# Kernel optimization log

Hardware: AMD Instinct MI355X
Metric: run time of the kernel (lower is better)

The kernel has to match this reference:

```python
import jax, jax.numpy as jnp
import numpy as np

EPS = 1e-5
K = 16
DILATION = 1

def _bn(x, g, b, axes):
    # BatchNorm in training mode: batch statistics over all axes except channel (last)
    m = jnp.mean(x, axis=axes, keepdims=True)
    v = jnp.var(x, axis=axes, keepdims=True)
    return (x - m) * jax.lax.rsqrt(v + EPS) * g + b

def _knn_idx(p, q, k):
    # p: [B,N,3], q: [B,M,3] -> indices [B,M,k] of nearest points in p for each q
    d = (jnp.sum(q * q, -1)[:, :, None]
         - 2.0 * jnp.einsum('bmc,bnc->bmn', q, p)
         + jnp.sum(p * p, -1)[:, None, :])  # [B,M,N]
    _, idx = jax.lax.top_k(-d, k)
    return jax.lax.stop_gradient(idx)

def setup_inputs() -> dict:
    key = jax.random.key(0)
    ks = jax.random.split(key, 16)
    B, N, M, Cin, Cout = 8, 8192, 2048, 64, 128
    mid, K2 = Cout // 4, K * K
    s = 0.02
    d = {
        'p': jax.random.normal(ks[0], (B, N, 3), jnp.float32),
        'q': jax.random.normal(ks[1], (B, M, 3), jnp.float32),
        'x': jax.random.normal(ks[2], (B, Cin, N), jnp.float32),
        # mlp: two 1x1 convs (3->mid->mid) each with BN
        'W1': jax.random.normal(ks[3], (mid, 3), jnp.float32) * s,
        'b1': jnp.zeros((mid,), jnp.float32),
        'g1': jnp.ones((mid,), jnp.float32), 'be1': jnp.zeros((mid,), jnp.float32),
        'W2': jax.random.normal(ks[4], (mid, mid), jnp.float32) * s,
        'b2': jnp.zeros((mid,), jnp.float32),
        'g2': jnp.ones((mid,), jnp.float32), 'be2': jnp.zeros((mid,), jnp.float32),
        # stn: conv [1,K] (3->K^2), then two 1x1 convs (K^2->K^2)
        'Ws1': jax.random.normal(ks[5], (K2, 3, K), jnp.float32) * s,
        'bs1': jnp.zeros((K2,), jnp.float32),
        'gs1': jnp.ones((K2,), jnp.float32), 'bes1': jnp.zeros((K2,), jnp.float32),
        'Ws2': jax.random.normal(ks[6], (K2, K2), jnp.float32) * s,
        'bs2': jnp.zeros((K2,), jnp.float32),
        'gs2': jnp.ones((K2,), jnp.float32), 'bes2': jnp.zeros((K2,), jnp.float32),
        'Ws3': jax.random.normal(ks[7], (K2, K2), jnp.float32) * s,
        'bs3': jnp.zeros((K2,), jnp.float32),
        # final conv [1,K]: (Cin+mid -> Cout) with BN
        'Wc': jax.random.normal(ks[8], (Cout, Cin + mid, K), jnp.float32) * s,
        'bc': jnp.zeros((Cout,), jnp.float32),
        'gc': jnp.ones((Cout,), jnp.float32), 'bec': jnp.zeros((Cout,), jnp.float32),
    }
    return d

def reference(p, q, x, W1, b1, g1, be1, W2, b2, g2, be2,
              Ws1, bs1, gs1, bes1, Ws2, bs2, gs2, bes2, Ws3, bs3,
              Wc, bc, gc, bec):
    B, M = q.shape[0], q.shape[1]
    idx = _knn_idx(p, q, K * DILATION)[..., ::DILATION]  # [B,M,K]
    # gather neighbor coords and center: p_hat [B,M,K,3]
    p_n = jax.vmap(lambda a, i: a[i])(p, idx)
    p_hat = p_n - q[:, :, None, :]
    # mlp (pointwise convs, channel-last)
    h = jax.nn.relu(_bn(jnp.einsum('bmkc,oc->bmko', p_hat, W1) + b1, g1, be1, (0, 1, 2)))
    h = jax.nn.relu(_bn(jnp.einsum('bmkc,oc->bmko', h, W2) + b2, g2, be2, (0, 1, 2)))
    # gather features: x [B,Cin,N] -> [B,M,K,Cin]
    xt = jnp.transpose(x, (0, 2, 1))
    x_n = jax.vmap(lambda a, i: a[i])(xt, idx)
    x_hat = jnp.concatenate([h, x_n], axis=-1)  # [B,M,K,mid+Cin]
    # stn -> transform T [B,M,K,K]
    t = jax.nn.relu(_bn(jnp.einsum('bmkc,ock->bmo', p_hat, Ws1) + bs1, gs1, bes1, (0, 1)))
    t = jax.nn.relu(_bn(jnp.einsum('bmi,oi->bmo', t, Ws2) + bs2, gs2, bes2, (0, 1)))
    t = jnp.einsum('bmi,oi->bmo', t, Ws3) + bs3  # [B,M,K*K]
    T = t.reshape(B, M, K, K)
    x2 = jnp.einsum('bmij,bmjc->bmic', T, x_hat)  # [B,M,K,mid+Cin]
    out = jax.nn.relu(_bn(jnp.einsum('bmkc,ock->bmo', x2, Wc) + bc, gc, bec, (0, 1)))  # [B,M,Cout]
    return (q, jnp.transpose(out, (0, 2, 1)))  # q, x:[B,Cout,M]
```

## Files before the change

kernel.cpp:

```cpp
#include <hip/hip_runtime.h>
#include <hip/hip_bf16.h>


#define EPS 1e-5f

constexpr int Bb   = 8;
constexpr int Np   = 8192;
constexpr int Mq   = 2048;
constexpr int COUT = 128;
constexpr int BM   = Bb * Mq;
constexpr int BMK  = BM * 16;
constexpr int GC   = 16;
constexpr int NC   = GC * GC * GC;
constexpr int CAP  = 320;

typedef __attribute__((ext_vector_type(8))) short short8;
typedef __attribute__((ext_vector_type(4))) float f32x4;

__device__ __forceinline__ unsigned short f2bf(float x) {
  unsigned u = __float_as_uint(x);
  u += 0x7fffu + ((u >> 16) & 1u);
  return (unsigned short)(u >> 16);
}
__device__ __forceinline__ float bf2f_lo(unsigned v) { return __uint_as_float(v << 16); }
__device__ __forceinline__ float bf2f_hi(unsigned v) { return __uint_as_float(v & 0xffff0000u); }

__device__ __forceinline__ int cell_of(float c) {
  int v = (int)floorf(c * 2.0f + 8.0f);
  return v < 0 ? 0 : (v > 15 ? 15 : v);
}

__device__ __forceinline__ unsigned enc_dist(float d) {
  unsigned uu = __float_as_uint(d);
  return uu ^ (((unsigned)(((int)uu) >> 31)) | 0x80000000u);
}

__device__ __forceinline__ void bsort64(unsigned long long& v, int lane) {
#pragma unroll
  for (int k = 2; k <= 64; k <<= 1) {
#pragma unroll
    for (int jj = k >> 1; jj > 0; jj >>= 1) {
      unsigned long long o = __shfl_xor(v, jj);
      bool keepMin = (((lane & k) == 0) == ((lane & jj) == 0));
      unsigned long long mn = v < o ? v : o;
      unsigned long long mx = v < o ? o : v;
      v = keepMin ? mn : mx;
    }
  }
}
__device__ __forceinline__ void bmerge64(unsigned long long& v, int lane) {
#pragma unroll
  for (int jj = 32; jj > 0; jj >>= 1) {
    unsigned long long o = __shfl_xor(v, jj);
    bool keepMin = ((lane & jj) == 0);
    unsigned long long mn = v < o ? v : o;
    unsigned long long mx = v < o ? o : v;
    v = keepMin ? mn : mx;
  }
}
__device__ __forceinline__ unsigned long long sort_smallest64(const unsigned long long* buf,
                                                              int C, int lane) {
  unsigned long long run = (lane < C) ? buf[lane] : ~0ULL;
  bsort64(run, lane);
  for (int b2 = 64; b2 < C; b2 += 64) {
    unsigned long long v = (b2 + lane < C) ? buf[b2 + lane] : ~0ULL;
    bsort64(v, lane);
    unsigned long long vr = __shfl_xor(v, 63);
    unsigned long long m = run < vr ? run : vr;
    bmerge64(m, lane);
    run = m;
  }
  return run;
}


__device__ __forceinline__ void bn1_compute(int o, const float* __restrict__ st,
                                            const float* __restrict__ W1,
                                            const float* __restrict__ b1,
                                            const float* __restrict__ g1,
                                            const float* __restrict__ be1,
                                            float* sc_out, float* shf_out) {
  float n = (float)BMK;
  float w0 = W1[3 * o], w1 = W1[3 * o + 1], w2 = W1[3 * o + 2], b = b1[o];
  float s0 = st[0], s1 = st[1], s2 = st[2];
  float m00 = st[3], m11 = st[4], m22 = st[5], m01 = st[6], m02 = st[7], m12 = st[8];
  float ws = (w0 * s0 + w1 * s1 + w2 * s2) / n;
  float mean = b + ws;
  float quad = w0 * w0 * m00 + w1 * w1 * m11 + w2 * w2 * m22 +
               2.f * (w0 * w1 * m01 + w0 * w2 * m02 + w1 * w2 * m12);
  float ex2 = quad / n + 2.f * b * ws + b * b;
  float var = ex2 - mean * mean;
  float sc = g1[o] * rsqrtf(var + EPS);
  *sc_out = sc;
  *shf_out = be1[o] - mean * sc + b * sc;
}

__global__ __launch_bounds__(256) void prep_kernel(const float* __restrict__ p,
                                                   const float* __restrict__ x,
                                                   const float* __restrict__ Wc,
                                                   const float* __restrict__ Ws1,
                                                   float4* __restrict__ pp4,
                                                   float* __restrict__ xt,
                                                   unsigned short* __restrict__ wcrp,
                                                   unsigned short* __restrict__ ws1r,
                                                   int* __restrict__ hist) {
  __shared__ float tile[64][65];
  int blk = blockIdx.x;
  int tid = threadIdx.x;
  if (blk < 256) {
    int i = blk * 256 + tid;
    float px = p[3 * i], py = p[3 * i + 1], pz = p[3 * i + 2];
    float pp = __fadd_rn(__fadd_rn(__fmul_rn(px, px), __fmul_rn(py, py)), __fmul_rn(pz, pz));
    pp4[i] = make_float4(px, py, pz, pp);
    int b = i >> 13;
    int cid = (cell_of(px) << 8) | (cell_of(py) << 4) | cell_of(pz);
    atomicAdd(&hist[b * NC + cid], 1);
  } else if (blk < 1280) {
    int bx = blk - 256;
    int b = bx >> 7;
    int n0 = (bx & 127) << 6;
    int nl = tid & 63;
    int r0 = tid >> 6;
    const float* xb = x + (size_t)b * 64 * Np;
    for (int c = r0; c < 64; c += 4) tile[c][nl] = xb[(size_t)c * Np + n0 + nl];
    __syncthreads();
    float* xtb = xt + (size_t)b * Np * 64;
    for (int n = r0; n < 64; n += 4) xtb[(size_t)(n0 + n) * 64 + nl] = tile[nl][n];
  } else if (blk < 2048) {
    int g = (blk - 1280) * 256 + tid;
    if (g < 128 * 1536) {
      int o = g / 1536, r = g % 1536;
      int c = r % 96, j = r / 96;
      wcrp[g] = f2bf(Wc[(size_t)o * 1536 + c * 16 + j]);
    }
  } else {
    int g = (blk - 2048) * 256 + tid;
    int o = g >> 6, i = g & 63;
    float val = 0.f;
    if (i < 48) {
      int k = i / 3, c = i - 3 * k;
      val = Ws1[(size_t)o * 48 + c * 16 + k];
    }
    unsigned short h = f2bf(val);
    float hf = __uint_as_float(((unsigned)h) << 16);
    unsigned short l = f2bf(val - hf);
    ws1r[g] = h;
    ws1r[16384 + g] = l;
  }
}

__global__ __launch_bounds__(256) void prefix_kernel(const int* __restrict__ hist,
                                                     int* __restrict__ cellstart,
                                                     int* __restrict__ cursor) {
  __shared__ int ls[256];
  int b = blockIdx.x, t = threadIdx.x;
  const int* h = hist + b * NC;
  int loc[16], s = 0;
#pragma unroll
  for (int k = 0; k < 16; ++k) { loc[k] = h[t * 16 + k]; s += loc[k]; }
  ls[t] = s;
  __syncthreads();
  for (int off = 1; off < 256; off <<= 1) {
    int v = (t >= off) ? ls[t - off] : 0;
    __syncthreads();
    ls[t] += v;
    __syncthreads();
  }
  int run = ls[t] - s;
  int* cs = cellstart + b * (NC + 1);
  int* cu = cursor + b * NC;
#pragma unroll
  for (int k = 0; k < 16; ++k) {
    cs[t * 16 + k] = run;
    cu[t * 16 + k] = run;
    run += loc[k];
  }
  if (t == 255) cs[NC] = run;
}

__global__ __launch_bounds__(256) void scatter_kernel(const float4* __restrict__ pp4,
                                                      int* __restrict__ cursor,
                                                      float4* __restrict__ sp4,
                                                      int* __restrict__ sidx) {
  int i = blockIdx.x * 256 + threadIdx.x;
  int b = i >> 13;
  float4 pv = pp4[i];
  int cid = (cell_of(pv.x) << 8) | (cell_of(pv.y) << 4) | cell_of(pv.z);
  int pos = atomicAdd(&cursor[b * NC + cid], 1);
  sp4[(size_t)b * Np + pos] = pv;
  sidx[(size_t)b * Np + pos] = i & 8191;
}

__global__ __launch_bounds__(256) void knn_kernel(const float4* __restrict__ pp4,
                                                  const float4* __restrict__ sp4,
                                                  const int* __restrict__ cellstart,
                                                  const float* __restrict__ q,
                                                  int* __restrict__ idx_out) {
  __shared__ unsigned long long cand[8][CAP];
  int tid = threadIdx.x;
  int wslot = tid >> 6;
  int wave = blockIdx.x * 4 + wslot;
  int lane = tid & 63;
  int q0 = wave * 2;
  int b = q0 >> 11;
  const float4* pb = pp4 + (size_t)b * Np;
  const float4* sp = sp4 + (size_t)b * Np;
  const int* cs = cellstart + b * (NC + 1);
  float qx[2], qy[2], qz[2], qqv[2];
#pragma unroll
  for (int j = 0; j < 2; ++j) {
    const float* qp = q + (size_t)(q0 + j) * 3;
    qx[j] = qp[0]; qy[j] = qp[1]; qz[j] = qp[2];
    qqv[j] = __fadd_rn(__fadd_rn(__fmul_rn(qx[j], qx[j]), __fmul_rn(qy[j], qy[j])),
                       __fmul_rn(qz[j], qz[j]));
  }
  float tau_f[2] = {INFINITY, INFINITY};

  for (int j = 0; j < 2; ++j) {
    int cx = cell_of(qx[j]), cy = cell_of(qy[j]), cz = cell_of(qz[j]);
    int alo = 0, blo = 0, nbw = 1, ncols = 1, zlo = 0, zhi = 0;
    int myS = 0, myE = 0;
    for (int r = 0;; ++r) {
      alo = cx - r; if (alo < 0) alo = 0;
      int ahi = cx + r; if (ahi > 15) ahi = 15;
      blo = cy - r; if (blo < 0) blo = 0;
      int bhi = cy + r; if (bhi > 15) bhi = 15;
      zlo = cz - r; if (zlo < 0) zlo = 0;
      zhi = cz + r; if (zhi > 15) zhi = 15;
      nbw = bhi - blo + 1;
      ncols = (ahi - alo + 1) * nbw;
      int total = 0;
      for (int l0 = 0; l0 < ncols; l0 += 64) {
        int l = l0 + lane;
        int sL = 0, eL = 0;
        if (l < ncols) {
          int da = l / nbw, db = l - da * nbw;
          int cbase = ((alo + da) << 8) | ((blo + db) << 4);
          sL = cs[cbase + zlo];
          eL = cs[cbase + zhi + 1];
        }
        if (l0 == 0) { myS = sL; myE = eL; }
        total += eL - sL;
      }
#pragma unroll
      for (int o = 32; o > 0; o >>= 1) total += __shfl_xor(total, o);
      if (total >= 16 || r >= 15) break;
    }
    unsigned u0 = 0xFFFFFFFFu, u1 = 0xFFFFFFFFu;
    int wcnt = 0;
    int ccen = (cx - alo) * nbw + (cy - blo);
    for (int c2 = 0; c2 < ncols && wcnt < 128; ++c2) {
      int cc = (c2 == 0) ? ccen : (c2 <= ccen ? c2 - 1 : c2);
      int s0, e;
      if (cc < 64) {
        s0 = __shfl(myS, cc);
        e = __shfl(myE, cc);
      } else {
        int da = cc / nbw, db = cc - da * nbw;
        int cbase = ((alo + da) << 8) | ((blo + db) << 4);
        s0 = cs[cbase + zlo];
        e = cs[cbase + zhi + 1];
      }
      for (int off = s0; off < e && wcnt < 128; off += 64) {
        int rem = e - off; if (rem > 64) rem = 64;
        int rot = wcnt & 63;
        int rel = (lane - rot) & 63;
        int g = wcnt + rel;
        if (rel < rem && g < 128) {
          float4 pv = sp[off + rel];
          float ee = __fmaf_rn(qz[j], pv.z, __fmaf_rn(qy[j], pv.y, __fmul_rn(qx[j], pv.x)));
          float d = __fadd_rn(__fsub_rn(qqv[j], __fmul_rn(2.0f, ee)), pv.w);
          unsigned uu = enc_dist(d);
          if (g < 64) u0 = uu; else u1 = uu;
        }
        wcnt += rem;
      }
    }
    unsigned lo = 0u, hi = 0xFF800000u;
    for (int it = 0; it < 20; ++it) {
      unsigned mid = lo + ((hi - lo) >> 1);
      int c = (int)__popcll(__ballot(u0 <= mid)) + (int)__popcll(__ballot(u1 <= mid));
      if (c >= 16) hi = mid; else lo = mid + 1;
    }
    tau_f[j] = (hi >= 0x80000000u) ? __uint_as_float(hi ^ 0x80000000u)
                                   : __uint_as_float(~hi);
  }

  int cnt[2] = {0, 0};
  unsigned long long lanebelow = (1ULL << lane) - 1ULL;
  for (int base = 0; base < Np; base += 256) {
    float4 pv[4];
#pragma unroll
    for (int u4 = 0; u4 < 4; ++u4) pv[u4] = pb[base + u4 * 64 + lane];
    float d[4][2];
#pragma unroll
    for (int u4 = 0; u4 < 4; ++u4)
#pragma unroll
      for (int j = 0; j < 2; ++j) {
        float e = __fmaf_rn(qz[j], pv[u4].z, __fmaf_rn(qy[j], pv[u4].y, __fmul_rn(qx[j], pv[u4].x)));
        d[u4][j] = __fadd_rn(__fsub_rn(qqv[j], __fmul_rn(2.0f, e)), pv[u4].w);
      }
#pragma unroll
    for (int u4 = 0; u4 < 4; ++u4)
#pragma unroll
      for (int j = 0; j < 2; ++j) {
        unsigned long long mask = __ballot(d[u4][j] <= tau_f[j]);
        if (mask) {
          if (d[u4][j] <= tau_f[j]) {
            int i = base + u4 * 64 + lane;
            unsigned uu = enc_dist(d[u4][j]);
            int wp = cnt[j] + (int)__popcll(mask & lanebelow);
            if (wp < CAP)
              cand[wslot * 2 + j][wp] = (((unsigned long long)uu) << 32) | (unsigned)i;
          }
          cnt[j] += (int)__popcll(mask);
        }
      }
  }
  __syncthreads();

  for (int j = 0; j < 2; ++j) {
    int slot = wslot * 2 + j;
    if (cnt[j] <= CAP) {
      unsigned long long run = sort_smallest64(&cand[slot][0], cnt[j], lane);
      if (lane < 16)
        idx_out[(size_t)(q0 + j) * 16 + lane] = (int)(run & 0xffffffffULL);
    } else {
      unsigned long long kk = ~0ULL;
      float tl = tau_f[j];
      for (int base = 0; base < Np; base += 64) {
        float4 pv = pb[base + lane];
        float ee = __fmaf_rn(qz[j], pv.z, __fmaf_rn(qy[j], pv.y, __fmul_rn(qx[j], pv.x)));
        float dv = __fadd_rn(__fsub_rn(qqv[j], __fmul_rn(2.0f, ee)), pv.w);
        unsigned long long mask = __ballot(dv <= tl);
        if (mask) {
          unsigned uu = enc_dist(dv);
          unsigned long long cd = (((unsigned long long)uu) << 32) | (unsigned)(base + lane);
          do {
            int src = __ffsll((unsigned long long)mask) - 1;
            mask &= mask - 1;
            unsigned long long ck = __shfl(cd, src);
            unsigned long long up = __shfl_up(kk, 1);
            if (lane == 0) up = 0ULL;
            if (lane < 16 && ck < kk) kk = (up > ck) ? up : ck;
          } while (mask);
          unsigned long long tt = __shfl(kk, 15);
          unsigned tm = (unsigned)(tt >> 32);
          unsigned inv2 = tm ^ ((tm & 0x80000000u) ? 0x80000000u : 0xFFFFFFFFu);
          float tc = (tm == 0xFFFFFFFFu) ? INFINITY : __uint_as_float(inv2);
          if (tc < tl) tl = tc;
        }
      }
      if (lane < 16)
        idx_out[(size_t)(q0 + j) * 16 + lane] = (int)(kk & 0xffffffffULL);
    }
  }
}

__global__ __launch_bounds__(256) void phat_stats_kernel(const float4* __restrict__ pp4,
                                                         const float* __restrict__ q,
                                                         const int* __restrict__ idx,
                                                         float* __restrict__ phat,
                                                         float* __restrict__ stats) {
  float a[9];
#pragma unroll
  for (int k = 0; k < 9; ++k) a[k] = 0.f;
  int tid = threadIdx.x;
  for (int it = 0; it < 4; ++it) {
    int bmk = blockIdx.x * 256 + tid + it * 65536;
    int bm = bmk >> 4;
    int b = bm >> 11;
    int j = idx[bmk];
    float4 pv = pp4[(size_t)b * Np + j];
    const float* qp = q + (size_t)bm * 3;
    float h0 = pv.x - qp[0], h1 = pv.y - qp[1], h2 = pv.z - qp[2];
    phat[(size_t)bmk * 3 + 0] = h0;
    phat[(size_t)bmk * 3 + 1] = h1;
    phat[(size_t)bmk * 3 + 2] = h2;
    a[0] += h0; a[1] += h1; a[2] += h2;
    a[3] += h0 * h0; a[4] += h1 * h1; a[5] += h2 * h2;
    a[6] += h0 * h1; a[7] += h0 * h2; a[8] += h1 * h2;
  }
#pragma unroll
  for (int off = 32; off > 0; off >>= 1)
#pragma unroll
    for (int k = 0; k < 9; ++k) a[k] += __shfl_down(a[k], off);
  __shared__ float ls[9];
  if (tid < 9) ls[tid] = 0.f;
  __syncthreads();
  if ((tid & 63) == 0)
    for (int k = 0; k < 9; ++k) atomicAdd(&ls[k], a[k]);
  __syncthreads();
  if (tid < 9) atomicAdd(&stats[tid], ls[tid]);
}

__global__ __launch_bounds__(256) void stats2_kernel(const float* __restrict__ phat,
                                                     const float* __restrict__ stats,
                                                     const float* __restrict__ W1,
                                                     const float* __restrict__ b1,
                                                     const float* __restrict__ g1,
                                                     const float* __restrict__ be1,
                                                     const float* __restrict__ W2,
                                                     const float* __restrict__ b2,
                                                     float* __restrict__ stats2) {
  __shared__ float hsh[256 * 36];
  __shared__ float w2s[32 * 33];
  __shared__ float w1s[96], sc1[32], sh1[32], b2s[32], ls[64];
  int tid = threadIdx.x;
  if (tid < 32) {
    bn1_compute(tid, stats, W1, b1, g1, be1, &sc1[tid], &sh1[tid]);
    b2s[tid] = b2[tid];
  }
  if (tid < 96) w1s[tid] = W1[tid];
  if (tid < 64) ls[tid] = 0.f;
  for (int e = tid; e < 1024; e += 256) w2s[(e >> 5) * 33 + (e & 31)] = W2[e];
  __syncthreads();
  {
    int bmk = blockIdx.x * 256 + tid;
    float h0 = phat[(size_t)bmk * 3], hy = phat[(size_t)bmk * 3 + 1], hz = phat[(size_t)bmk * 3 + 2];
#pragma unroll
    for (int o4 = 0; o4 < 8; ++o4) {
      float4 r;
      float* rp = (float*)&r;
#pragma unroll
      for (int u = 0; u < 4; ++u) {
        int o = o4 * 4 + u;
        float t = w1s[3 * o] * h0 + w1s[3 * o + 1] * hy + w1s[3 * o + 2] * hz;
        rp[u] = fmaxf(0.f, t * sc1[o] + sh1[o]);
      }
      *(float4*)&hsh[tid * 36 + o4 * 4] = r;
    }
  }
  __syncthreads();
  int oc = tid & 31, grp = tid >> 5;
  float wrow[32];
#pragma unroll
  for (int c = 0; c < 32; ++c) wrow[c] = w2s[oc * 33 + c];
  float bias = b2s[oc];
  float ss = 0.f, qq = 0.f;
  for (int r = 0; r < 32; ++r) {
    int row = grp * 32 + r;
    float a = bias;
    const float4* hr = (const float4*)&hsh[row * 36];
#pragma unroll
    for (int c4 = 0; c4 < 8; ++c4) {
      float4 hv = hr[c4];
      a += hv.x * wrow[c4 * 4 + 0];
      a += hv.y * wrow[c4 * 4 + 1];
      a += hv.z * wrow[c4 * 4 + 2];
      a += hv.w * wrow[c4 * 4 + 3];
    }
    ss += a;
    qq += a * a;
  }
  atomicAdd(&ls[oc], ss);
  atomicAdd(&ls[32 + oc], qq);
  __syncthreads();
  if (tid < 64) atomicAdd(&stats2[tid], ls[tid]);
}

__global__ __launch_bounds__(256) void stn1_kernel(const float* __restrict__ phat,
                                                   const unsigned short* __restrict__ ws1r,
                                                   const float* __restrict__ bs1,
                                                   float* __restrict__ pt1,
                                                   float* __restrict__ spt1) {
  __shared__ unsigned short Ah[64 * 72], Al[64 * 72], Bh[128 * 72], Bl[128 * 72];
  __shared__ float ls[256];
  int tid = threadIdx.x;
  ls[tid] = 0.f;
  int mb = blockIdx.x >> 1, nb = blockIdx.x & 1;
  int bm0 = mb * 64, o0 = nb * 128;
  {
    int zr = tid >> 2, zc = 48 + (tid & 3) * 4;
    *(unsigned long long*)&Ah[zr * 72 + zc] = 0ULL;
    *(unsigned long long*)&Al[zr * 72 + zc] = 0ULL;
  }
  {
    int ar = tid >> 2, aseg = tid & 3;
    const float* Ap = phat + (size_t)(bm0 + ar) * 48 + aseg * 12;
    float4 v0 = *(const float4*)(Ap);
    float4 v1 = *(const float4*)(Ap + 4);
    float4 v2 = *(const float4*)(Ap + 8);
    float av[12] = {v0.x, v0.y, v0.z, v0.w, v1.x, v1.y, v1.z, v1.w, v2.x, v2.y, v2.z, v2.w};
    unsigned long long ph[3] = {0ULL, 0ULL, 0ULL}, pl[3] = {0ULL, 0ULL, 0ULL};
#pragma unroll
    for (int t = 0; t < 12; ++t) {
      unsigned short h = f2bf(av[t]);
      float hf = __uint_as_float(((unsigned)h) << 16);
      unsigned short l = f2bf(av[t] - hf);
      ph[t >> 2] |= ((unsigned long long)h) << ((t & 3) * 16);
      pl[t >> 2] |= ((unsigned long long)l) << ((t & 3) * 16);
    }
    int base = ar * 72 + aseg * 12;
#pragma unroll
    for (int t4 = 0; t4 < 3; ++t4) {
      *(unsigned long long*)&Ah[base + t4 * 4] = ph[t4];
      *(unsigned long long*)&Al[base + t4 * 4] = pl[t4];
    }
  }
#pragma unroll
  for (int pass = 0; pass < 4; ++pass) {
    int g = pass * 2048 + tid * 8;
    int br = g >> 6, i2 = g & 63;
    short8 vh = *(const short8*)&ws1r[(size_t)(o0 + br) * 64 + i2];
    short8 vl = *(const short8*)&ws1r[16384 + (size_t)(o0 + br) * 64 + i2];
    *(short8*)&Bh[br * 72 + i2] = vh;
    *(short8*)&Bl[br * 72 + i2] = vl;
  }
  __syncthreads();
  int wid = tid >> 6, lane = tid & 63;
  int wm = wid >> 1, wn = wid & 1;
  int mh = lane & 15, quad = lane >> 4;
  f32x4 acc[2][4];
#pragma unroll
  for (int a = 0; a < 2; ++a)
#pragma unroll
    for (int bq = 0; bq < 4; ++bq) acc[a][bq] = (f32x4){0.f, 0.f, 0.f, 0.f};
#pragma unroll
  for (int kc = 0; kc < 2; ++kc) {
    int ko = kc * 32 + quad * 8;
#pragma unroll
    for (int mt = 0; mt < 2; ++mt) {
      short8 ah = *(const short8*)&Ah[(wm * 32 + mt * 16 + mh) * 72 + ko];
      short8 al = *(const short8*)&Al[(wm * 32 + mt * 16 + mh) * 72 + ko];
#pragma unroll
      for (int nt = 0; nt < 4; ++nt) {
        short8 bh = *(const short8*)&Bh[(wn * 64 + nt * 16 + mh) * 72 + ko];
        short8 bl = *(const short8*)&Bl[(wn * 64 + nt * 16 + mh) * 72 + ko];
        acc[mt][nt] = __builtin_amdgcn_mfma_f32_16x16x32_bf16(ah, bh, acc[mt][nt], 0, 0, 0);
        acc[mt][nt] = __builtin_amdgcn_mfma_f32_16x16x32_bf16(ah, bl, acc[mt][nt], 0, 0, 0);
        acc[mt][nt] = __builtin_amdgcn_mfma_f32_16x16x32_bf16(al, bh, acc[mt][nt], 0, 0, 0);
      }
    }
  }
#pragma unroll
  for (int mt = 0; mt < 2; ++mt)
#pragma unroll
    for (int nt = 0; nt < 4; ++nt) {
      int colL = wn * 64 + nt * 16 + mh;
      int col = o0 + colL;
      float bvv = bs1[col];
      float ps = 0.f, pq = 0.f;
#pragma unroll
      for (int r = 0; r < 4; ++r) {
        float val = acc[mt][nt][r] + bvv;
        pt1[(size_t)(bm0 + wm * 32 + mt * 16 + quad * 4 + r) * 256 + col] = val;
        ps += val;
        pq += val * val;
      }
      atomicAdd(&ls[colL], ps);
      atomicAdd(&ls[128 + colL], pq);
    }
  __syncthreads();
  if (tid < 128) {
    atomicAdd(&spt1[o0 + tid], ls[tid]);
    atomicAdd(&spt1[256 + o0 + tid], ls[128 + tid]);
  }
}

__global__ __launch_bounds__(256) void stn_mm_kernel(const float* __restrict__ in,
                                                     const float* __restrict__ sums,
                                                     const float* __restrict__ gg,
                                                     const float* __restrict__ be,
                                                     const float* __restrict__ W,
                                                     const float* __restrict__ bias,
                                                     float* __restrict__ out,
                                                     float* __restrict__ outstats,
                                                     int do_stats) {
  __shared__ unsigned short As[64 * 40], Bs[128 * 40];
  __shared__ float scA[256], shA[256], ls[256];
  int tid = threadIdx.x;
  ls[tid] = 0.f;
  {
    float n = (float)BM;
    float mean = sums[tid] / n;
    float var = sums[256 + tid] / n - mean * mean;
    float s = gg[tid] * rsqrtf(var + EPS);
    scA[tid] = s;
    shA[tid] = be[tid] - mean * s;
  }
  int mb = blockIdx.x >> 1, nb = blockIdx.x & 1;
  int bm0 = mb * 64, o0 = nb * 128;
  int wid = tid >> 6, lane = tid & 63;
  int wm = wid >> 1, wn = wid & 1;
  int mh = lane & 15, quad = lane >> 4;
  f32x4 acc[2][4];
#pragma unroll
  for (int a = 0; a < 2; ++a)
#pragma unroll
    for (int bq = 0; bq < 4; ++bq) acc[a][bq] = (f32x4){0.f, 0.f, 0.f, 0.f};
  int ar = tid >> 2, aseg = tid & 3;
  const float* Ag = in + (size_t)(bm0 + ar) * 256 + aseg * 8;
  int aoff = ar * 40 + aseg * 8;
  int ci = aseg * 8;
  for (int i0 = 0; i0 < 256; i0 += 32) {
    __syncthreads();
    float4 v0 = *(const float4*)(Ag + i0);
    float4 v1 = *(const float4*)(Ag + i0 + 4);
    float av[8] = {v0.x, v0.y, v0.z, v0.w, v1.x, v1.y, v1.z, v1.w};
    short8 ap;
#pragma unroll
    for (int k = 0; k < 8; ++k)
      ap[k] = (short)f2bf(fmaxf(0.f, av[k] * scA[i0 + ci + k] + shA[i0 + ci + k]));
    *(short8*)&As[aoff] = ap;
#pragma unroll
    for (int jb = 0; jb < 2; ++jb) {
      int br = jb * 64 + ar;
      const float* Bg = W + (size_t)(o0 + br) * 256 + aseg * 8;
      float4 u0 = *(const float4*)(Bg + i0);
      float4 u1 = *(const float4*)(Bg + i0 + 4);
      float bv[8] = {u0.x, u0.y, u0.z, u0.w, u1.x, u1.y, u1.z, u1.w};
      short8 bp;
#pragma unroll
      for (int k = 0; k < 8; ++k) bp[k] = (short)f2bf(bv[k]);
      *(short8*)&Bs[br * 40 + aseg * 8] = bp;
    }
    __syncthreads();
#pragma unroll
    for (int mt = 0; mt < 2; ++mt) {
      short8 af = *(const short8*)&As[(wm * 32 + mt * 16 + mh) * 40 + quad * 8];
#pragma unroll
      for (int nt = 0; nt < 4; ++nt) {
        short8 bf = *(const short8*)&Bs[(wn * 64 + nt * 16 + mh) * 40 + quad * 8];
        acc[mt][nt] = __builtin_amdgcn_mfma_f32_16x16x32_bf16(af, bf, acc[mt][nt], 0, 0, 0);
      }
    }
  }
#pragma unroll
  for (int mt = 0; mt < 2; ++mt)
#pragma unroll
    for (int nt = 0; nt < 4; ++nt) {
      int colL = wn * 64 + nt * 16 + mh;
      int col = o0 + colL;
      float bvv = bias[col];
      float ps = 0.f, pq = 0.f;
#pragma unroll
      for (int r = 0; r < 4; ++r) {
        float val = acc[mt][nt][r] + bvv;
        out[(size_t)(bm0 + wm * 32 + mt * 16 + quad * 4 + r) * 256 + col] = val;
        ps += val;
        pq += val * val;
      }
      if (do_stats) {
        atomicAdd(&ls[colL], ps);
        atomicAdd(&ls[128 + colL], pq);
      }
    }
  if (do_stats) {
    __syncthreads();
    if (tid < 128) {
      atomicAdd(&outstats[o0 + tid], ls[tid]);
      atomicAdd(&outstats[256 + o0 + tid], ls[128 + tid]);
    }
  }
}

__global__ __launch_bounds__(256) void xhat_x2_kernel(const float* __restrict__ phat,
                                                      const float* __restrict__ stats,
                                                      const float* __restrict__ stats2,
                                                      const float* __restrict__ W1,
                                                      const float* __restrict__ b1,
                                                      const float* __restrict__ g1,
                                                      const float* __restrict__ be1,
                                                      const float* __restrict__ W2,
                                                      const float* __restrict__ b2,
                                                      const float* __restrict__ g2,
                                                      const float* __restrict__ be2,
                                                      const float* __restrict__ xt,
                                                      const int* __restrict__ idx,
                                                      const float* __restrict__ Tbuf,
                                                      unsigned short* __restrict__ x2) {
  __shared__ unsigned short xh[256 * 98];
  __shared__ float w1s[96], w2s[32 * 33], sc1[32], sh1[32], sc2[32], sh2[32];
  int tid = threadIdx.x;
  if (tid < 32) {
    bn1_compute(tid, stats, W1, b1, g1, be1, &sc1[tid], &sh1[tid]);
    float n = (float)BMK;
    float mean = stats2[tid] / n;
    float var = stats2[32 + tid] / n - mean * mean;
    float s = g2[tid] * rsqrtf(var + EPS);
    sc2[tid] = s;
    sh2[tid] = be2[tid] - mean * s + b2[tid] * s;
  }
  if (tid < 96) w1s[tid] = W1[tid];
  for (int e = tid; e < 1024; e += 256) w2s[(e >> 5) * 33 + (e & 31)] = W2[e];
  __syncthreads();
  int bm0 = blockIdx.x * 16;
  int b = bm0 >> 11;
  int bml = tid >> 4, j = tid & 15;
  int bmk = (bm0 + bml) * 16 + j;
  int row = tid * 98;
  {
    float h0 = phat[(size_t)bmk * 3], hy = phat[(size_t)bmk * 3 + 1], hz = phat[(size_t)bmk * 3 + 2];
    float h1[32];
#pragma unroll
    for (int o = 0; o < 32; ++o) {
      float t = w1s[3 * o] * h0 + w1s[3 * o + 1] * hy + w1s[3 * o + 2] * hz;
      h1[o] = fmaxf(0.f, t * sc1[o] + sh1[o]);
    }
#pragma unroll
    for (int o4 = 0; o4 < 8; ++o4) {
      float r[4];
#pragma unroll
      for (int u = 0; u < 4; ++u) {
        int o = o4 * 4 + u;
        float a = 0.f;
#pragma unroll
        for (int c = 0; c < 32; ++c) a += h1[c] * w2s[o * 33 + c];
        r[u] = fmaxf(0.f, a * sc2[o] + sh2[o]);
      }
      *(unsigned*)&xh[row + o4 * 4] = (unsigned)f2bf(r[0]) | (((unsigned)f2bf(r[1])) << 16);
      *(unsigned*)&xh[row + o4 * 4 + 2] = (unsigned)f2bf(r[2]) | (((unsigned)f2bf(r[3])) << 16);
    }
    int jx = idx[bmk];
    const float4* xr = (const float4*)(xt + ((size_t)b * Np + jx) * 64);
#pragma unroll
    for (int c4 = 0; c4 < 16; ++c4) {
      float4 v = xr[c4];
      *(unsigned*)&xh[row + 32 + c4 * 4] = (unsigned)f2bf(v.x) | (((unsigned)f2bf(v.y)) << 16);
      *(unsigned*)&xh[row + 32 + c4 * 4 + 2] = (unsigned)f2bf(v.z) | (((unsigned)f2bf(v.w)) << 16);
    }
  }
  float Tr[16];
  {
    const float4* tg = (const float4*)(Tbuf + (size_t)(bm0 + bml) * 256 + j * 16);
#pragma unroll
    for (int w4 = 0; w4 < 4; ++w4) {
      float4 tv = tg[w4];
      Tr[w4 * 4 + 0] = tv.x; Tr[w4 * 4 + 1] = tv.y;
      Tr[w4 * 4 + 2] = tv.z; Tr[w4 * 4 + 3] = tv.w;
    }
  }
  __syncthreads();
#pragma unroll
  for (int c0 = 0; c0 < 96; c0 += 32) {
    float acc[32];
#pragma unroll
    for (int cc = 0; cc < 32; ++cc) acc[cc] = 0.f;
#pragma unroll
    for (int jj = 0; jj < 16; ++jj) {
      const unsigned* xr2 = (const unsigned*)&xh[(bml * 16 + jj) * 98 + c0];
      float t = Tr[jj];
#pragma unroll
      for (int cc = 0; cc < 16; ++cc) {
        unsigned uv = xr2[cc];
        acc[cc * 2] += t * bf2f_lo(uv);
        acc[cc * 2 + 1] += t * bf2f_hi(uv);
      }
    }
    unsigned* dst = (unsigned*)(x2 + (size_t)bmk * 96 + c0);
#pragma unroll
    for (int cc = 0; cc < 16; ++cc)
      dst[cc] = (unsigned)f2bf(acc[cc * 2]) | (((unsigned)f2bf(acc[cc * 2 + 1])) << 16);
  }
}

__global__ __launch_bounds__(256) void preout_kernel(const unsigned short* __restrict__ x2,
                                                     const unsigned short* __restrict__ Wcrp,
                                                     const float* __restrict__ bc,
                                                     float* __restrict__ pout,
                                                     float* __restrict__ spout) {
  __shared__ unsigned short As[64 * 40], Bs[128 * 40];
  __shared__ float ls[256];
  int tid = threadIdx.x;
  ls[tid] = 0.f;
  int bm0 = blockIdx.x * 64;
  int wid = tid >> 6, lane = tid & 63;
  int wm = wid >> 1, wn = wid & 1;
  int mh = lane & 15, quad = lane >> 4;
  f32x4 acc[2][4];
#pragma unroll
  for (int a = 0; a < 2; ++a)
#pragma unroll
    for (int bq = 0; bq < 4; ++bq) acc[a][bq] = (f32x4){0.f, 0.f, 0.f, 0.f};
  int ar = tid >> 2, aseg = tid & 3;
  const unsigned short* Ag = x2 + (size_t)(bm0 + ar) * 1536 + aseg * 8;
  const unsigned short* Bg0 = Wcrp + (size_t)ar * 1536 + aseg * 8;
  const unsigned short* Bg1 = Wcrp + (size_t)(64 + ar) * 1536 + aseg * 8;
  int aoff = ar * 40 + aseg * 8;
  short8 a_pre = *(const short8*)Ag;
  short8 b_pre0 = *(const short8*)Bg0;
  short8 b_pre1 = *(const short8*)Bg1;
  for (int i0 = 0; i0 < 1536; i0 += 32) {
    __syncthreads();
    *(short8*)&As[aoff] = a_pre;
    *(short8*)&Bs[aoff] = b_pre0;
    *(short8*)&Bs[64 * 40 + aoff] = b_pre1;
    __syncthreads();
    if (i0 + 32 < 1536) {
      a_pre = *(const short8*)(Ag + i0 + 32);
      b_pre0 = *(const short8*)(Bg0 + i0 + 32);
      b_pre1 = *(const short8*)(Bg1 + i0 + 32);
    }
#pragma unroll
    for (int mt = 0; mt < 2; ++mt) {
      short8 af = *(const short8*)&As[(wm * 32 + mt * 16 + mh) * 40 + quad * 8];
#pragma unroll
      for (int nt = 0; nt < 4; ++nt) {
        short8 bf = *(const short8*)&Bs[(wn * 64 + nt * 16 + mh) * 40 + quad * 8];
        acc[mt][nt] = __builtin_amdgcn_mfma_f32_16x16x32_bf16(af, bf, acc[mt][nt], 0, 0, 0);
      }
    }
  }
#pragma unroll
  for (int mt = 0; mt < 2; ++mt)
#pragma unroll
    for (int nt = 0; nt < 4; ++nt) {
      int col = wn * 64 + nt * 16 + mh;
      float bvv = bc[col];
      float ps = 0.f, pq = 0.f;
#pragma unroll
      for (int r = 0; r < 4; ++r) {
        float val = acc[mt][nt][r] + bvv;
        pout[(size_t)(bm0 + wm * 32 + mt * 16 + quad * 4 + r) * 128 + col] = val;
        ps += val;
        pq += val * val;
      }
      atomicAdd(&ls[col], ps);
      atomicAdd(&ls[128 + col], pq);
    }
  __syncthreads();
  atomicAdd(&spout[tid], ls[tid]);
}

__global__ __launch_bounds__(256) void final_kernel(const float* __restrict__ q,
                                                    const float* __restrict__ pout,
                                                    const float* __restrict__ scs,
                                                    const float* __restrict__ gc,
                                                    const float* __restrict__ bec,
                                                    float* __restrict__ dout) {
  __shared__ float ldsT[128 * 65];
  int blk = blockIdx.x;
  int tid = threadIdx.x;
  if (blk < 192) {
    int g = blk * 256 + tid;
    dout[g] = q[g];
    return;
  }
  int blk2 = blk - 192;
  int b = blk2 >> 5;
  int m0 = (blk2 & 31) * 64;
  int row = tid >> 2, seg = tid & 3;
  const float4* src = (const float4*)(pout + ((size_t)(b * Mq) + m0 + row) * 128 + seg * 32);
#pragma unroll
  for (int k4 = 0; k4 < 8; ++k4) {
    float4 v = src[k4];
    int o = seg * 32 + k4 * 4;
    ldsT[(o + 0) * 65 + row] = v.x;
    ldsT[(o + 1) * 65 + row] = v.y;
    ldsT[(o + 2) * 65 + row] = v.z;
    ldsT[(o + 3) * 65 + row] = v.w;
  }
  __syncthreads();
  int lane = tid & 63, wv = tid >> 6;
  float n = (float)BM;
  float* base = dout + (size_t)BM * 3 + (size_t)b * COUT * Mq + m0;
#pragma unroll
  for (int rep = 0; rep < 32; ++rep) {
    int o = wv * 32 + rep;
    float mean = scs[o] / n;
    float var = scs[128 + o] / n - mean * mean;
    float s = gc[o] * rsqrtf(var + EPS);
    float shv = bec[o] - mean * s;
    float v = ldsT[o * 65 + lane];
    base[(size_t)o * Mq + lane] = fmaxf(0.f, v * s + shv);
  }
}

extern "C" void kernel_launch(void* const* d_in, const int* in_sizes, int n_in, void* d_out,
                              int out_size, void* d_ws, size_t ws_size, hipStream_t stream) {
  const float* p = (const float*)d_in[0];
  const float* q = (const float*)d_in[1];
  const float* x = (const float*)d_in[2];
  const float* W1 = (const float*)d_in[3];
  const float* b1 = (const float*)d_in[4];
  const float* g1 = (const float*)d_in[5];
  const float* be1 = (const float*)d_in[6];
  const float* W2 = (const float*)d_in[7];
  const float* b2 = (const float*)d_in[8];
  const float* g2 = (const float*)d_in[9];
  const float* be2 = (const float*)d_in[10];
  const float* Ws1 = (const float*)d_in[11];
  const float* bs1 = (const float*)d_in[12];
  const float* gs1 = (const float*)d_in[13];
  const float* bes1 = (const float*)d_in[14];
  const float* Ws2 = (const float*)d_in[15];
  const float* bs2 = (const float*)d_in[16];
  const float* gs2 = (const float*)d_in[17];
  const float* bes2 = (const float*)d_in[18];
  const float* Ws3 = (const float*)d_in[19];
  const float* bs3 = (const float*)d_in[20];
  const float* Wc = (const float*)d_in[21];
  const float* bc = (const float*)d_in[22];
  const float* gc = (const float*)d_in[23];
  const float* bec = (const float*)d_in[24];
  float* dout = (float*)d_out;

  char* ws = (char*)d_ws;
  float* stats = (float*)ws;
  size_t off = 8192;
  float4* pp4 = (float4*)(ws + off);  off += (size_t)Bb * Np * 16;
  int* idxb = (int*)(ws + off);       off += (size_t)BMK * 4;
  float* xt = (float*)(ws + off);     off += (size_t)Bb * Np * 64 * 4;
  float* phat = (float*)(ws + off);   off += (size_t)BMK * 3 * 4;
  float* pt1 = (float*)(ws + off);    off += (size_t)BM * 256 * 4;
  float* pt2 = (float*)(ws + off);    off += (size_t)BM * 256 * 4;
  float* Tb = (float*)(ws + off);     off += (size_t)BM * 256 * 4;
  float* pout = (float*)(ws + off);   off += (size_t)BM * 128 * 4;
  unsigned short* wcrp = (unsigned short*)(ws + off); off += (size_t)1536 * 128 * 2;
  unsigned short* x2 = (unsigned short*)(ws + off);   off += (size_t)BM * 1536 * 2;
  int* hist = (int*)(ws + off);       off += (size_t)Bb * NC * 4;
  int* cursor = (int*)(ws + off);     off += (size_t)Bb * NC * 4;
  int* cellstart = (int*)(ws + off);  off += (size_t)Bb * (NC + 1) * 4;
  float4* sp4 = (float4*)(ws + off);  off += (size_t)Bb * Np * 16;
  int* sidx = (int*)(ws + off);       off += (size_t)Bb * Np * 4;
  unsigned short* ws1r = (unsigned short*)(ws + off); off += (size_t)2 * 256 * 64 * 2;

  hipMemsetAsync(stats, 0, 8192, stream);
  hipMemsetAsync(hist, 0, (size_t)Bb * NC * 4, stream);
  hipLaunchKernelGGL(prep_kernel, dim3(2112), dim3(256), 0, stream, p, x, Wc, Ws1, pp4, xt, wcrp, ws1r, hist);
  hipLaunchKernelGGL(prefix_kernel, dim3(8), dim3(256), 0, stream, hist, cellstart, cursor);
  hipLaunchKernelGGL(scatter_kernel, dim3(256), dim3(256), 0, stream, pp4, cursor, sp4, sidx);
  hipLaunchKernelGGL(knn_kernel, dim3(2048), dim3(256), 0, stream, pp4, sp4, cellstart, q, idxb);
  hipLaunchKernelGGL(phat_stats_kernel, dim3(256), dim3(256), 0, stream, pp4, q, idxb, phat, stats);
  hipLaunchKernelGGL(stn1_kernel, dim3(512), dim3(256), 0, stream, phat, ws1r, bs1, pt1, stats + 128);
  hipLaunchKernelGGL(stats2_kernel, dim3(1024), dim3(256), 0, stream, phat, stats, W1, b1, g1, be1, W2, b2, stats + 16);
  hipLaunchKernelGGL(stn_mm_kernel, dim3(512), dim3(256), 0, stream, pt1, stats + 128, gs1, bes1, Ws2, bs2, pt2, stats + 640, 1);
  hipLaunchKernelGGL(stn_mm_kernel, dim3(512), dim3(256), 0, stream, pt2, stats + 640, gs2, bes2, Ws3, bs3, Tb, (float*)nullptr, 0);
  hipLaunchKernelGGL(xhat_x2_kernel, dim3(1024), dim3(256), 0, stream, phat, stats, stats + 16,
                     W1, b1, g1, be1, W2, b2, g2, be2, xt, idxb, Tb, x2);
  hipLaunchKernelGGL(preout_kernel, dim3(256), dim3(256), 0, stream, x2, wcrp, bc, pout, stats + 1152);
  hipLaunchKernelGGL(final_kernel, dim3(448), dim3(256), 0, stream, q, pout, stats + 1152, gc, bec, dout);
}
```

Baseline: 381.1 us.

## Restrict KNN candidate scan to grid cells within threshold radius; shrink xhat LDS

The second KNN pass no longer scans all 8192 points per query. It computes a radius from the per-query threshold and visits only the sorted grid cells inside that bounding box, then maps each hit back to its original index through sidx. Separately, xhat_x2 now stages one 32-channel chunk at a time into a smaller padded LDS buffer, keeping h2 in registers and loading the x gather per chunk. The first part should remove most of the brute-force distance work. The costs are reliance on the radius padding being conservative, per-column shuffle overhead, and extra block barriers in xhat_x2.

Measured after the change: 379.9 us. No clear change (-0.3%).

```diff
diff --git a/kernel.cpp b/kernel.cpp
--- a/kernel.cpp
+++ b/kernel.cpp
@@ -193,6 +193,7 @@
 
 __global__ __launch_bounds__(256) void knn_kernel(const float4* __restrict__ pp4,
                                                   const float4* __restrict__ sp4,
+                                                  const int* __restrict__ sidx,
                                                   const int* __restrict__ cellstart,
                                                   const float* __restrict__ q,
                                                   int* __restrict__ idx_out) {
@@ -205,6 +206,7 @@
   int b = q0 >> 11;
   const float4* pb = pp4 + (size_t)b * Np;
   const float4* sp = sp4 + (size_t)b * Np;
+  const int* sx = sidx + (size_t)b * Np;
   const int* cs = cellstart + b * (NC + 1);
   float qx[2], qy[2], qz[2], qqv[2];
 #pragma unroll
@@ -288,34 +290,51 @@
 
   int cnt[2] = {0, 0};
   unsigned long long lanebelow = (1ULL << lane) - 1ULL;
-  for (int base = 0; base < Np; base += 256) {
-    float4 pv[4];
-#pragma unroll
-    for (int u4 = 0; u4 < 4; ++u4) pv[u4] = pb[base + u4 * 64 + lane];
-    float d[4][2];
-#pragma unroll
-    for (int u4 = 0; u4 < 4; ++u4)
-#pragma unroll
-      for (int j = 0; j < 2; ++j) {
-        float e = __fmaf_rn(qz[j], pv[u4].z, __fmaf_rn(qy[j], pv[u4].y, __fmul_rn(qx[j], pv[u4].x)));
-        d[u4][j] = __fadd_rn(__fsub_rn(qqv[j], __fmul_rn(2.0f, e)), pv[u4].w);
-      }
-#pragma unroll
-    for (int u4 = 0; u4 < 4; ++u4)
-#pragma unroll
-      for (int j = 0; j < 2; ++j) {
-        unsigned long long mask = __ballot(d[u4][j] <= tau_f[j]);
+  for (int j = 0; j < 2; ++j) {
+    float R = sqrtf(fmaxf(tau_f[j], 0.f) + 3e-5f) * 1.0005f;
+    int ax0 = cell_of(qx[j] - R), ax1 = cell_of(qx[j] + R);
+    int ay0 = cell_of(qy[j] - R), ay1 = cell_of(qy[j] + R);
+    int az0 = cell_of(qz[j] - R), az1 = cell_of(qz[j] + R);
+    int nby = ay1 - ay0 + 1;
+    int ncols = (ax1 - ax0 + 1) * nby;
+    int myS = 0, myE = 0;
+    if (lane < ncols) {
+      int da = lane / nby, db = lane - da * nby;
+      int cbase = ((ax0 + da) << 8) | ((ay0 + db) << 4);
+      myS = cs[cbase + az0];
+      myE = cs[cbase + az1 + 1];
+    }
+    for (int cc = 0; cc < ncols; ++cc) {
+      int s0, e;
+      if (cc < 64) {
+        s0 = __shfl(myS, cc);
+        e = __shfl(myE, cc);
+      } else {
+        int da = cc / nby, db = cc - da * nby;
+        int cbase = ((ax0 + da) << 8) | ((ay0 + db) << 4);
+        s0 = cs[cbase + az0];
+        e = cs[cbase + az1 + 1];
+      }
+      for (int off = s0; off < e; off += 64) {
+        int pos = off + lane;
+        bool valid = pos < e;
+        float4 pv = sp[valid ? pos : s0];
+        float ee = __fmaf_rn(qz[j], pv.z, __fmaf_rn(qy[j], pv.y, __fmul_rn(qx[j], pv.x)));
+        float d = __fadd_rn(__fsub_rn(qqv[j], __fmul_rn(2.0f, ee)), pv.w);
+        if (!valid) d = __uint_as_float(0x7FC00000u);
+        unsigned long long mask = __ballot(d <= tau_f[j]);
         if (mask) {
-          if (d[u4][j] <= tau_f[j]) {
-            int i = base + u4 * 64 + lane;
-            unsigned uu = enc_dist(d[u4][j]);
+          if (d <= tau_f[j]) {
+            int oi = sx[pos];
+            unsigned uu = enc_dist(d);
             int wp = cnt[j] + (int)__popcll(mask & lanebelow);
             if (wp < CAP)
-              cand[wslot * 2 + j][wp] = (((unsigned long long)uu) << 32) | (unsigned)i;
+              cand[wslot * 2 + j][wp] = (((unsigned long long)uu) << 32) | (unsigned)oi;
           }
           cnt[j] += (int)__popcll(mask);
         }
       }
+    }
   }
   __syncthreads();
 
@@ -670,7 +689,7 @@
                                                       const int* __restrict__ idx,
                                                       const float* __restrict__ Tbuf,
                                                       unsigned short* __restrict__ x2) {
-  __shared__ unsigned short xh[256 * 98];
+  __shared__ unsigned xh[256 * 17];
   __shared__ float w1s[96], w2s[32 * 33], sc1[32], sh1[32], sc2[32], sh2[32];
   int tid = threadIdx.x;
   if (tid < 32) {
@@ -689,14 +708,14 @@
   int b = bm0 >> 11;
   int bml = tid >> 4, j = tid & 15;
   int bmk = (bm0 + bml) * 16 + j;
-  int row = tid * 98;
+  unsigned h2p[16];
   {
     float h0 = phat[(size_t)bmk * 3], hy = phat[(size_t)bmk * 3 + 1], hz = phat[(size_t)bmk * 3 + 2];
-    float h1[32];
+    float h1v[32];
 #pragma unroll
     for (int o = 0; o < 32; ++o) {
       float t = w1s[3 * o] * h0 + w1s[3 * o + 1] * hy + w1s[3 * o + 2] * hz;
-      h1[o] = fmaxf(0.f, t * sc1[o] + sh1[o]);
+      h1v[o] = fmaxf(0.f, t * sc1[o] + sh1[o]);
     }
 #pragma unroll
     for (int o4 = 0; o4 < 8; ++o4) {
@@ -706,21 +725,15 @@
         int o = o4 * 4 + u;
         float a = 0.f;
 #pragma unroll
-        for (int c = 0; c < 32; ++c) a += h1[c] * w2s[o * 33 + c];
+        for (int c = 0; c < 32; ++c) a += h1v[c] * w2s[o * 33 + c];
         r[u] = fmaxf(0.f, a * sc2[o] + sh2[o]);
       }
-      *(unsigned*)&xh[row + o4 * 4] = (unsigned)f2bf(r[0]) | (((unsigned)f2bf(r[1])) << 16);
-      *(unsigned*)&xh[row + o4 * 4 + 2] = (unsigned)f2bf(r[2]) | (((unsigned)f2bf(r[3])) << 16);
-    }
-    int jx = idx[bmk];
-    const float4* xr = (const float4*)(xt + ((size_t)b * Np + jx) * 64);
-#pragma unroll
-    for (int c4 = 0; c4 < 16; ++c4) {
-      float4 v = xr[c4];
-      *(unsigned*)&xh[row + 32 + c4 * 4] = (unsigned)f2bf(v.x) | (((unsigned)f2bf(v.y)) << 16);
-      *(unsigned*)&xh[row + 32 + c4 * 4 + 2] = (unsigned)f2bf(v.z) | (((unsigned)f2bf(v.w)) << 16);
-    }
-  }
+      h2p[o4 * 2] = (unsigned)f2bf(r[0]) | (((unsigned)f2bf(r[1])) << 16);
+      h2p[o4 * 2 + 1] = (unsigned)f2bf(r[2]) | (((unsigned)f2bf(r[3])) << 16);
+    }
+  }
+  int jx = idx[bmk];
+  const float4* xr = (const float4*)(xt + ((size_t)b * Np + jx) * 64);
   float Tr[16];
   {
     const float4* tg = (const float4*)(Tbuf + (size_t)(bm0 + bml) * 256 + j * 16);
@@ -731,15 +744,29 @@
       Tr[w4 * 4 + 2] = tv.z; Tr[w4 * 4 + 3] = tv.w;
     }
   }
-  __syncthreads();
-#pragma unroll
-  for (int c0 = 0; c0 < 96; c0 += 32) {
+  unsigned* dst32 = (unsigned*)(x2 + (size_t)bmk * 96);
+#pragma unroll
+  for (int ch = 0; ch < 3; ++ch) {
+    if (ch == 0) {
+#pragma unroll
+      for (int t = 0; t < 16; ++t) xh[tid * 17 + t] = h2p[t];
+    } else {
+      float4 xv[8];
+#pragma unroll
+      for (int t = 0; t < 8; ++t) xv[t] = xr[(ch - 1) * 8 + t];
+#pragma unroll
+      for (int t = 0; t < 8; ++t) {
+        xh[tid * 17 + t * 2] = (unsigned)f2bf(xv[t].x) | (((unsigned)f2bf(xv[t].y)) << 16);
+        xh[tid * 17 + t * 2 + 1] = (unsigned)f2bf(xv[t].z) | (((unsigned)f2bf(xv[t].w)) << 16);
+      }
+    }
+    __syncthreads();
     float acc[32];
 #pragma unroll
     for (int cc = 0; cc < 32; ++cc) acc[cc] = 0.f;
 #pragma unroll
     for (int jj = 0; jj < 16; ++jj) {
-      const unsigned* xr2 = (const unsigned*)&xh[(bml * 16 + jj) * 98 + c0];
+      const unsigned* xr2 = &xh[(bml * 16 + jj) * 17];
       float t = Tr[jj];
 #pragma unroll
       for (int cc = 0; cc < 16; ++cc) {
@@ -748,10 +775,10 @@
         acc[cc * 2 + 1] += t * bf2f_hi(uv);
       }
     }
-    unsigned* dst = (unsigned*)(x2 + (size_t)bmk * 96 + c0);
 #pragma unroll
     for (int cc = 0; cc < 16; ++cc)
-      dst[cc] = (unsigned)f2bf(acc[cc * 2]) | (((unsigned)f2bf(acc[cc * 2 + 1])) << 16);
+      dst32[ch * 16 + cc] = (unsigned)f2bf(acc[cc * 2]) | (((unsigned)f2bf(acc[cc * 2 + 1])) << 16);
+    __syncthreads();
   }
 }
 
@@ -921,7 +948,7 @@
   hipLaunchKernelGGL(prep_kernel, dim3(2112), dim3(256), 0, stream, p, x, Wc, Ws1, pp4, xt, wcrp, ws1r, hist);
   hipLaunchKernelGGL(prefix_kernel, dim3(8), dim3(256), 0, stream, hist, cellstart, cursor);
   hipLaunchKernelGGL(scatter_kernel, dim3(256), dim3(256), 0, stream, pp4, cursor, sp4, sidx);
-  hipLaunchKernelGGL(knn_kernel, dim3(2048), dim3(256), 0, stream, pp4, sp4, cellstart, q, idxb);
+  hipLaunchKernelGGL(knn_kernel, dim3(2048), dim3(256), 0, stream, pp4, sp4, sidx, cellstart, q, idxb);
   hipLaunchKernelGGL(phat_stats_kernel, dim3(256), dim3(256), 0, stream, pp4, q, idxb, phat, stats);
   hipLaunchKernelGGL(stn1_kernel, dim3(512), dim3(256), 0, stream, phat, ws1r, bs1, pt1, stats + 128);
   hipLaunchKernelGGL(stats2_kernel, dim3(1024), dim3(256), 0, stream, phat, stats, W1, b1, g1, be1, W2, b2, stats + 16);
```
